# Performance work log

Measured on AMD Instinct MI355X. Metric: run time of the kernel, lower is better.

The kernel has to match this reference:

```python
import jax, jax.numpy as jnp
import numpy as np
from jax import lax

VOCAB = 100000; E = 512; HID = 1024; H = HID // 2; T = 7; L = 4096
START = 4; STOP = 5; NEG = -10000.0


def setup_inputs() -> dict:
    key = jax.random.key(0)
    ks = jax.random.split(key, 14)
    s = 0.05  # ~1/sqrt(H), matches torch default init scale
    transitions = jax.random.normal(ks[12], (T, T), dtype=jnp.float32)
    transitions = transitions.at[START, :].set(NEG).at[:, STOP].set(NEG)
    return {
        "sentence": jax.random.randint(ks[0], (L,), 0, VOCAB),
        "emb": jax.random.normal(ks[1], (VOCAB, E), dtype=jnp.float32) * s,
        "w_ih_f": jax.random.normal(ks[2], (4 * H, E), dtype=jnp.float32) * s,
        "w_hh_f": jax.random.normal(ks[3], (4 * H, H), dtype=jnp.float32) * s,
        "b_ih_f": jax.random.normal(ks[4], (4 * H,), dtype=jnp.float32) * s,
        "b_hh_f": jax.random.normal(ks[5], (4 * H,), dtype=jnp.float32) * s,
        "w_ih_b": jax.random.normal(ks[6], (4 * H, E), dtype=jnp.float32) * s,
        "w_hh_b": jax.random.normal(ks[7], (4 * H, H), dtype=jnp.float32) * s,
        "b_ih_b": jax.random.normal(ks[8], (4 * H,), dtype=jnp.float32) * s,
        "b_hh_b": jax.random.normal(ks[9], (4 * H,), dtype=jnp.float32) * s,
        "w_out": jax.random.normal(ks[10], (T, HID), dtype=jnp.float32) * s,
        "b_out": jax.random.normal(ks[11], (T,), dtype=jnp.float32) * s,
        "transitions": transitions,
    }


def _lstm_dir(x, w_ih, w_hh, b_ih, b_hh):
    # x: [L, E] -> hidden states [L, H]; zero initial state (torch default)
    xg = x @ w_ih.T + b_ih  # [L, 4H] precomputed input gates
    h0 = jnp.zeros((H,), x.dtype)
    c0 = jnp.zeros((H,), x.dtype)
    def step(carry, g):
        h, c = carry
        gates = g + w_hh @ h + b_hh
        i, f, gg, o = jnp.split(gates, 4)
        i = jax.nn.sigmoid(i); f = jax.nn.sigmoid(f)
        gg = jnp.tanh(gg); o = jax.nn.sigmoid(o)
        c = f * c + i * gg
        h = o * jnp.tanh(c)
        return (h, c), h
    _, hs = lax.scan(step, (h0, c0), xg)
    return hs


def reference(sentence, emb, w_ih_f, w_hh_f, b_ih_f, b_hh_f,
              w_ih_b, w_hh_b, b_ih_b, b_hh_b, w_out, b_out, transitions):
    x = emb[sentence]  # [L, E]
    hf = _lstm_dir(x, w_ih_f, w_hh_f, b_ih_f, b_hh_f)            # [L, H]
    hb = _lstm_dir(x[::-1], w_ih_b, w_hh_b, b_ih_b, b_hh_b)[::-1]
    feats = jnp.concatenate([hf, hb], axis=1) @ w_out.T + b_out  # [L, T]

    # Viterbi max-plus DP
    init = jnp.full((T,), NEG, feats.dtype).at[START].set(0.0)
    def vstep(fv, feat):
        sc = fv[None, :] + transitions           # [next, prev]
        bp = jnp.argmax(sc, axis=1)
        return jnp.max(sc, axis=1) + feat, bp
    fv, bptrs = lax.scan(vstep, init, feats)     # bptrs: [L, T]
    terminal = fv + transitions[STOP]
    best = jnp.argmax(terminal)
    score = terminal[best]
    # backtrack
    def bt(tag, bp):
        return bp[tag], tag
    _, path_rev = lax.scan(bt, best, bptrs[::-1])
    best_path = path_rev[::-1]                   # [L] tag ids
    return best_path, score
```

## Files before the change

### kernel.cpp

```cpp
#include <hip/hip_runtime.h>
#include <hip/hip_bf16.h>

#define L     4096
#define E     512
#define HID   1024
#define HH    512
#define G4    2048
#define T_TAG 7
#define START_TAG 4
#define STOP_TAG  5
#define NEGV  (-10000.0f)

#define NWRK  32
#define NHELP 224
#define NTILE (64 * 2 * 32)
#define SENT  0xFFFFFFFFu

__device__ __forceinline__ float aload_f(const float* p) {
    const unsigned int v = __hip_atomic_load((const unsigned int*)p,
                                             __ATOMIC_RELAXED,
                                             __HIP_MEMORY_SCOPE_AGENT);
    return __uint_as_float(v);
}
__device__ __forceinline__ void astore_f(float* p, float x) {
    __hip_atomic_store((unsigned int*)p, __float_as_uint(x),
                       __ATOMIC_RELAXED, __HIP_MEMORY_SCOPE_AGENT);
}

__global__ __launch_bounds__(512)
void fused_kernel(const int* __restrict__ sentence, const float* __restrict__ emb,
                  const float* __restrict__ wih_f, const float* __restrict__ bih_f,
                  const float* __restrict__ bhh_f,
                  const float* __restrict__ wih_b, const float* __restrict__ bih_b,
                  const float* __restrict__ bhh_b,
                  const float* __restrict__ whh_f, const float* __restrict__ whh_b,
                  const float* __restrict__ wout, const float* __restrict__ bout,
                  float* __restrict__ xg_f, float* __restrict__ xg_b,
                  float* __restrict__ hf, float* __restrict__ hb,
                  float* __restrict__ feats, int* cnt)
{
    const int bid = blockIdx.x;
    const int tid = threadIdx.x;

    __shared__ float h_lds[2][HH];
    __shared__ float glds[8][16];
    __shared__ float As[32][68];
    __shared__ float Bs[32][68];
    __shared__ int   sent_s[64];
    __shared__ float red_s[8][8];

    if (bid < NWRK) {
        const int dir = bid >> 4;
        const int rnk = bid & 15;

        const float* __restrict__ xg  = dir ? xg_b  : xg_f;
        const float* __restrict__ whh = dir ? whh_b : whh_f;
        float* __restrict__ hout = dir ? hb : hf;

        const int wave = tid >> 6;
        const int lane = tid & 63;
        const int g    = wave >> 1;
        const int jh   = wave & 1;
        const int u0   = rnk * 32;

        float w[16][8];
#pragma unroll
        for (int rr = 0; rr < 16; rr++) {
            const size_t row = (size_t)(g * HH + u0 + jh * 16 + rr);
#pragma unroll
            for (int k = 0; k < 8; k++)
                w[rr][k] = whh[row * HH + (size_t)(k * 64 + lane)];
        }

        float c_state = 0.f;
        const int uu = u0 + (tid & 31);

        auto wait_chunk = [&](int tc) {
            const int* cp = cnt + dir * 64 + tc;
            while (__hip_atomic_load(cp, __ATOMIC_ACQUIRE,
                                     __HIP_MEMORY_SCOPE_AGENT) < 32) {
                __builtin_amdgcn_s_sleep(1);
            }
        };

        float xq0 = 0.f, xq1 = 0.f, xq2 = 0.f, xq3 = 0.f;
        if (tid < 32) {
            wait_chunk(dir ? 63 : 0);
            const float* xgt = xg + (size_t)(dir ? (L - 1) : 0) * G4;
            xq0 = aload_f(xgt + uu);            xq1 = aload_f(xgt + HH + uu);
            xq2 = aload_f(xgt + 2 * HH + uu);   xq3 = aload_f(xgt + 3 * HH + uu);
        }

        for (int s = 0; s < L; s++) {
            const int t = dir ? (L - 1 - s) : s;
            const int p = s & 1;

            unsigned int v = 0;
            if (s > 0) {
                const int tp = dir ? (t + 1) : (t - 1);
                const unsigned int* hp =
                    (const unsigned int*)(hout + (size_t)tp * HH) + tid;
                do {
                    v = __hip_atomic_load(hp, __ATOMIC_RELAXED,
                                          __HIP_MEMORY_SCOPE_AGENT);
                } while (v == SENT);
            }
            h_lds[p][tid] = __uint_as_float(v);
            __syncthreads();

            float hv[8];
#pragma unroll
            for (int k = 0; k < 8; k++) hv[k] = h_lds[p][k * 64 + lane];

            float acc[16];
#pragma unroll
            for (int rr = 0; rr < 16; rr++) {
                float a = 0.f;
#pragma unroll
                for (int k = 0; k < 8; k++) a += w[rr][k] * hv[k];
                acc[rr] = a;
            }

            {
                const bool b0 = lane & 1;
#pragma unroll
                for (int r = 0; r < 8; r++) {
                    const float send = b0 ? acc[r] : acc[r + 8];
                    const float recv = __shfl_xor(send, 1, 64);
                    acc[r] = (b0 ? acc[r + 8] : acc[r]) + recv;
                }
                const bool b1 = lane & 2;
#pragma unroll
                for (int r = 0; r < 4; r++) {
                    const float send = b1 ? acc[r] : acc[r + 4];
                    const float recv = __shfl_xor(send, 2, 64);
                    acc[r] = (b1 ? acc[r + 4] : acc[r]) + recv;
                }
                const bool b2 = lane & 4;
#pragma unroll
                for (int r = 0; r < 2; r++) {
                    const float send = b2 ? acc[r] : acc[r + 2];
                    const float recv = __shfl_xor(send, 4, 64);
                    acc[r] = (b2 ? acc[r + 2] : acc[r]) + recv;
                }
                const bool b3 = lane & 8;
                {
                    const float send = b3 ? acc[0] : acc[1];
                    const float recv = __shfl_xor(send, 8, 64);
                    acc[0] = (b3 ? acc[1] : acc[0]) + recv;
                }
                acc[0] += __shfl_xor(acc[0], 16, 64);
                acc[0] += __shfl_xor(acc[0], 32, 64);
            }
            if (lane < 16) {
                const int R = ((lane & 1) << 3) | ((lane & 2) << 1) |
                              ((lane & 4) >> 1) | ((lane & 8) >> 3);
                glds[wave][R] = acc[0];
            }
            __syncthreads();

            if (tid < 32) {
                const int jh_ = tid >> 4;
                const int rr  = tid & 15;
                float iv = glds[0 + jh_][rr] + xq0;
                float fv = glds[2 + jh_][rr] + xq1;
                float gv = glds[4 + jh_][rr] + xq2;
                float ov = glds[6 + jh_][rr] + xq3;
                iv = 1.f / (1.f + expf(-iv));
                fv = 1.f / (1.f + expf(-fv));
                gv = tanhf(gv);
                ov = 1.f / (1.f + expf(-ov));
                c_state = fv * c_state + iv * gv;
                const float hval = ov * tanhf(c_state);
                __hip_atomic_store((unsigned int*)&hout[(size_t)t * HH + uu],
                                   __float_as_uint(hval), __ATOMIC_RELAXED,
                                   __HIP_MEMORY_SCOPE_AGENT);
                if (s + 1 < L) {
                    const int tn = dir ? (t - 1) : (t + 1);
                    if ((tn & 63) == (dir ? 63 : 0)) wait_chunk(tn >> 6);
                    const float* xgt = xg + (size_t)tn * G4;
                    xq0 = aload_f(xgt + uu);
                    xq1 = aload_f(xgt + HH + uu);
                    xq2 = aload_f(xgt + 2 * HH + uu);
                    xq3 = aload_f(xgt + 3 * HH + uu);
                }
            }
        }
        return;
    }

    const int hid_ = bid - NWRK;

    for (int tile = hid_; tile < NTILE; tile += NHELP) {
        const int jt = tile & 31;
        const int sd = tile >> 5;
        const int dr = sd & 1;
        const int sc = sd >> 1;
        const int t0 = dr ? (L - 64 - sc * 64) : (sc * 64);
        const int j0 = jt * 64;
        const float* __restrict__ wih = dr ? wih_b : wih_f;
        const float* __restrict__ bih = dr ? bih_b : bih_f;
        const float* __restrict__ bhh = dr ? bhh_b : bhh_f;
        float* __restrict__ xg = dr ? xg_b : xg_f;

        if (tid < 64) sent_s[tid] = sentence[t0 + tid];

        const int li = tid >> 3;
        const int k4 = (tid & 7) * 4;
        const int tx = tid & 15;
        const int ty = tid >> 4;

        float a00 = 0.f, a01 = 0.f, a02 = 0.f, a03 = 0.f;
        float a10 = 0.f, a11 = 0.f, a12 = 0.f, a13 = 0.f;

        for (int k0 = 0; k0 < E; k0 += 32) {
            __syncthreads();
            {
                const float4 av = *(const float4*)(emb + (size_t)sent_s[li] * E + k0 + k4);
                As[k4 + 0][li] = av.x; As[k4 + 1][li] = av.y;
                As[k4 + 2][li] = av.z; As[k4 + 3][li] = av.w;
                const float4 bv = *(const float4*)(wih + (size_t)(j0 + li) * E + k0 + k4);
                Bs[k4 + 0][li] = bv.x; Bs[k4 + 1][li] = bv.y;
                Bs[k4 + 2][li] = bv.z; Bs[k4 + 3][li] = bv.w;
            }
            __syncthreads();
#pragma unroll
            for (int k = 0; k < 32; k++) {
                const float a0 = As[k][ty * 2 + 0];
                const float a1 = As[k][ty * 2 + 1];
                const float4 b4 = *(const float4*)&Bs[k][tx * 4];
                a00 += a0 * b4.x; a01 += a0 * b4.y; a02 += a0 * b4.z; a03 += a0 * b4.w;
                a10 += a1 * b4.x; a11 += a1 * b4.y; a12 += a1 * b4.z; a13 += a1 * b4.w;
            }
        }

        {
            const int c0 = j0 + tx * 4;
            const float bsum0 = bih[c0 + 0] + bhh[c0 + 0];
            const float bsum1 = bih[c0 + 1] + bhh[c0 + 1];
            const float bsum2 = bih[c0 + 2] + bhh[c0 + 2];
            const float bsum3 = bih[c0 + 3] + bhh[c0 + 3];
            float* r0 = xg + (size_t)(t0 + ty * 2 + 0) * G4 + c0;
            float* r1 = xg + (size_t)(t0 + ty * 2 + 1) * G4 + c0;
            astore_f(r0 + 0, a00 + bsum0); astore_f(r0 + 1, a01 + bsum1);
            astore_f(r0 + 2, a02 + bsum2); astore_f(r0 + 3, a03 + bsum3);
            astore_f(r1 + 0, a10 + bsum0); astore_f(r1 + 1, a11 + bsum1);
            astore_f(r1 + 2, a12 + bsum2); astore_f(r1 + 3, a13 + bsum3);
        }
        __syncthreads();
        if (tid == 0)
            __hip_atomic_fetch_add(&cnt[dr * 64 + (t0 >> 6)], 1,
                                   __ATOMIC_RELEASE, __HIP_MEMORY_SCOPE_AGENT);
    }

    const int wave = tid >> 6, lane = tid & 63;
    for (int t = hid_; t < L; t += NHELP) {
        if (tid < 32) {
            const float* src = (tid < 16) ? hf : hb;
            const unsigned int* wp =
                (const unsigned int*)(src + (size_t)t * HH) + (tid & 15) * 32;
            while (__hip_atomic_load(wp, __ATOMIC_RELAXED,
                                     __HIP_MEMORY_SCOPE_AGENT) == SENT) {
                __builtin_amdgcn_s_sleep(8);
            }
        }
        __syncthreads();

        const unsigned int* p0 = (const unsigned int*)(hf + (size_t)t * HH) + tid;
        const unsigned int* p1 = (const unsigned int*)(hb + (size_t)t * HH) + tid;
        unsigned int v0, v1;
        do { v0 = __hip_atomic_load(p0, __ATOMIC_RELAXED,
                                    __HIP_MEMORY_SCOPE_AGENT); } while (v0 == SENT);
        do { v1 = __hip_atomic_load(p1, __ATOMIC_RELAXED,
                                    __HIP_MEMORY_SCOPE_AGENT); } while (v1 == SENT);
        const float x0 = __uint_as_float(v0);
        const float x1 = __uint_as_float(v1);

        float acc[T_TAG];
#pragma unroll
        for (int i = 0; i < T_TAG; i++)
            acc[i] = x0 * wout[i * HID + tid] + x1 * wout[i * HID + HH + tid];
#pragma unroll
        for (int m = 1; m < 64; m <<= 1) {
#pragma unroll
            for (int i = 0; i < T_TAG; i++) acc[i] += __shfl_xor(acc[i], m, 64);
        }
        if (lane == 0) {
#pragma unroll
            for (int i = 0; i < T_TAG; i++) red_s[wave][i] = acc[i];
        }
        __syncthreads();
        if (tid < T_TAG) {
            float ssum = bout[tid];
#pragma unroll
            for (int wv = 0; wv < 8; wv++) ssum += red_s[wv][tid];
            feats[(size_t)t * 8 + tid] = ssum;
        }
        __syncthreads();
    }
}

__global__ __launch_bounds__(64)
void viterbi_kernel(const float* __restrict__ feats, const float* __restrict__ trans,
                    float* __restrict__ out)
{
    __shared__ unsigned char bp[L][8];
    __shared__ unsigned char gl[64][8];
    __shared__ unsigned char bnd[64];

    const int tid = threadIdx.x;

    float tr[T_TAG][T_TAG];
#pragma unroll
    for (int i = 0; i < T_TAG; i++)
#pragma unroll
        for (int j = 0; j < T_TAG; j++) tr[i][j] = trans[i * T_TAG + j];

    const int d = tid % T_TAG;
    float trd[T_TAG];
#pragma unroll
    for (int j = 0; j < T_TAG; j++) trd[j] = trans[d * T_TAG + j];

    float trS[T_TAG];
#pragma unroll
    for (int j = 0; j < T_TAG; j++) trS[j] = trans[STOP_TAG * T_TAG + j];

    float fv0 = NEGV, fv1 = NEGV, fv2 = NEGV, fv3 = NEGV,
          fv4 = 0.f,  fv5 = NEGV, fv6 = NEGV;

    float4 qa[8], qb[8];
#pragma unroll
    for (int q = 0; q < 8; q++) {
        qa[q] = *(const float4*)(feats + (size_t)q * 8);
        qb[q] = *(const float4*)(feats + (size_t)q * 8 + 4);
    }

#define VMAXROW(I, OUT, FI)                                                    \
    {                                                                          \
        const float a0 = fv0 + tr[I][0], a1 = fv1 + tr[I][1];                  \
        const float a2 = fv2 + tr[I][2], a3 = fv3 + tr[I][3];                  \
        const float a4 = fv4 + tr[I][4], a5 = fv5 + tr[I][5];                  \
        const float a6 = fv6 + tr[I][6];                                       \
        const float m012 = fmaxf(fmaxf(a0, a1), a2);                           \
        const float m345 = fmaxf(fmaxf(a3, a4), a5);                           \
        OUT = fmaxf(fmaxf(m012, m345), a6) + (FI);                             \
    }

#define VSTEP(T, Q, PRE)                                                       \
    {                                                                          \
        const float4 fa = qa[Q], fb = qb[Q];                                   \
                     \
        {                                                                      \
            float bv_ = fv0 + trd[0]; int bj_ = 0; float c_;                   \
            c_ = fv1 + trd[1]; if (c_ > bv_) { bv_ = c_; bj_ = 1; }            \
            c_ = fv2 + trd[2]; if (c_ > bv_) { bv_ = c_; bj_ = 2; }            \
            c_ = fv3 + trd[3]; if (c_ > bv_) { bv_ = c_; bj_ = 3; }            \
            c_ = fv4 + trd[4]; if (c_ > bv_) { bv_ = c_; bj_ = 4; }            \
            c_ = fv5 + trd[5]; if (c_ > bv_) { bv_ = c_; bj_ = 5; }            \
            c_ = fv6 + trd[6]; if (c_ > bv_) { bv_ = c_; bj_ = 6; }            \
            if (tid < T_TAG) bp[(T)][tid] = (unsigned char)bj_;                \
        }                                                                      \
                 \
        float nf0, nf1, nf2, nf3, nf4, nf5, nf6;                               \
        VMAXROW(0, nf0, fa.x) VMAXROW(1, nf1, fa.y) VMAXROW(2, nf2, fa.z)      \
        VMAXROW(3, nf3, fa.w) VMAXROW(4, nf4, fb.x) VMAXROW(5, nf5, fb.y)      \
        VMAXROW(6, nf6, fb.z)                                                  \
        fv0 = nf0; fv1 = nf1; fv2 = nf2; fv3 = nf3;                            \
        fv4 = nf4; fv5 = nf5; fv6 = nf6;                                       \
        if (PRE) {                                                             \
            qa[Q] = *(const float4*)(feats + (size_t)((T) + 8) * 8);           \
            qb[Q] = *(const float4*)(feats + (size_t)((T) + 8) * 8 + 4);       \
        }                                                                      \
    }

    for (int tb = 0; tb < L - 8; tb += 8) {
#pragma unroll
        for (int q = 0; q < 8; q++) VSTEP(tb + q, q, true)
    }
    {
        const int tb = L - 8;
#pragma unroll
        for (int q = 0; q < 8; q++) VSTEP(tb + q, q, false)
    }
#undef VSTEP
#undef VMAXROW

    int bt_final; float best_score;
    {
        float bv_ = fv0 + trS[0]; int bj_ = 0; float c_;
        c_ = fv1 + trS[1]; if (c_ > bv_) { bv_ = c_; bj_ = 1; }
        c_ = fv2 + trS[2]; if (c_ > bv_) { bv_ = c_; bj_ = 2; }
        c_ = fv3 + trS[3]; if (c_ > bv_) { bv_ = c_; bj_ = 3; }
        c_ = fv4 + trS[4]; if (c_ > bv_) { bv_ = c_; bj_ = 4; }
        c_ = fv5 + trS[5]; if (c_ > bv_) { bv_ = c_; bj_ = 5; }
        c_ = fv6 + trS[6]; if (c_ > bv_) { bv_ = c_; bj_ = 6; }
        bt_final = bj_; best_score = bv_;
    }
    __syncthreads();

    const int lo = 64 * tid + 1;
    const int hi = (tid == 63) ? (L - 1) : (64 * tid + 64);
    {
        unsigned int c0 = 0, c1 = 1, c2 = 2, c3 = 3, c4 = 4, c5 = 5, c6 = 6;
        for (int t = hi; t >= lo; --t) {
            const unsigned char* row = &bp[t][0];
            c0 = row[c0]; c1 = row[c1]; c2 = row[c2]; c3 = row[c3];
            c4 = row[c4]; c5 = row[c5]; c6 = row[c6];
        }
        gl[tid][0] = (unsigned char)c0; gl[tid][1] = (unsigned char)c1;
        gl[tid][2] = (unsigned char)c2; gl[tid][3] = (unsigned char)c3;
        gl[tid][4] = (unsigned char)c4; gl[tid][5] = (unsigned char)c5;
        gl[tid][6] = (unsigned char)c6;
    }
    __syncthreads();

    if (tid == 0) {
        int b = bt_final;
        for (int l2 = 63; l2 >= 0; --l2) {
            bnd[l2] = (unsigned char)b;
            b = gl[l2][b];
        }
    }
    __syncthreads();

    {
        int tag = bnd[tid];
        for (int t = hi; t >= lo; --t) {
            tag = bp[t][tag];
            out[t - 1] = (float)tag;
        }
    }
    if (tid == 63) {
        out[L - 1] = (float)bt_final;
        out[L]     = best_score;
    }
}

extern "C" void kernel_launch(void* const* d_in, const int* in_sizes, int n_in,
                              void* d_out, int out_size, void* d_ws, size_t ws_size,
                              hipStream_t stream)
{
    const int*   sentence = (const int*)  d_in[0];
    const float* emb      = (const float*)d_in[1];
    const float* wih_f    = (const float*)d_in[2];
    const float* whh_f    = (const float*)d_in[3];
    const float* bih_f    = (const float*)d_in[4];
    const float* bhh_f    = (const float*)d_in[5];
    const float* wih_b    = (const float*)d_in[6];
    const float* whh_b    = (const float*)d_in[7];
    const float* bih_b    = (const float*)d_in[8];
    const float* bhh_b    = (const float*)d_in[9];
    const float* wout     = (const float*)d_in[10];
    const float* bout     = (const float*)d_in[11];
    const float* trans    = (const float*)d_in[12];
    float* out = (float*)d_out;

    char* ws = (char*)d_ws;
    int*   cnt    = (int*)ws;
    float* xg_f   = (float*)(ws + 1024);
    float* xg_b   = xg_f  + (size_t)L * G4;
    float* hfbuf  = xg_b  + (size_t)L * G4;
    float* hbbuf  = hfbuf + (size_t)L * HH;
    float* featsb = hbbuf + (size_t)L * HH;

    hipMemsetAsync(cnt, 0, 1024, stream);
    hipMemsetAsync(hfbuf, 0xFF, (size_t)2 * L * HH * sizeof(float), stream);

    void* args[] = { (void*)&sentence, (void*)&emb,
                     (void*)&wih_f, (void*)&bih_f, (void*)&bhh_f,
                     (void*)&wih_b, (void*)&bih_b, (void*)&bhh_b,
                     (void*)&whh_f, (void*)&whh_b,
                     (void*)&wout, (void*)&bout,
                     (void*)&xg_f, (void*)&xg_b,
                     (void*)&hfbuf, (void*)&hbbuf,
                     (void*)&featsb, (void*)&cnt };
    hipLaunchCooperativeKernel((void*)fused_kernel, dim3(NWRK + NHELP),
                               dim3(512), args, 0, stream);

    hipLaunchKernelGGL(viterbi_kernel, dim3(1), dim3(64), 0, stream,
                       featsb, trans, out);
}
```

Baseline: 9.102 ms.

## Fuse Viterbi into persistent kernel as dedicated block streaming feats via sentinels

Moves the Viterbi forward pass and backtrack into one block of the cooperative kernel. That block polls the feats buffer, which is pre-filled with a sentinel value, and double-buffers 32 timesteps at a time in LDS, so the DP overlaps the LSTM and feature computation instead of running after it in a second kernel launch. Shared memory becomes a union across the roles to fit the bp table, and one helper block is given up. The feats stores become atomic stores and the memset grows to cover feats. The trade-off is one fewer GEMM helper and spin-polling traffic from the Viterbi block.

```diff
diff --git a/kernel.cpp b/kernel.cpp
--- a/kernel.cpp
+++ b/kernel.cpp
@@ -12,20 +12,30 @@
 #define NEGV  (-10000.0f)
 
 #define NWRK  32
-#define NHELP 224
+#define VITB  32
+#define NHELP 223
 #define NTILE (64 * 2 * 32)
 #define SENT  0xFFFFFFFFu
 
+__device__ __forceinline__ unsigned int aload_u(const float* p) {
+    return __hip_atomic_load((const unsigned int*)p, __ATOMIC_RELAXED,
+                             __HIP_MEMORY_SCOPE_AGENT);
+}
 __device__ __forceinline__ float aload_f(const float* p) {
-    const unsigned int v = __hip_atomic_load((const unsigned int*)p,
-                                             __ATOMIC_RELAXED,
-                                             __HIP_MEMORY_SCOPE_AGENT);
-    return __uint_as_float(v);
+    return __uint_as_float(aload_u(p));
 }
 __device__ __forceinline__ void astore_f(float* p, float x) {
     __hip_atomic_store((unsigned int*)p, __float_as_uint(x),
                        __ATOMIC_RELAXED, __HIP_MEMORY_SCOPE_AGENT);
 }
+
+union SMem {
+    struct { float h_lds[2][HH]; float glds[8][16]; } wk;
+    struct { float As[32][68]; float Bs[32][68]; int sent[64];
+             float red[8][8]; } hp;
+    struct { unsigned char bp[L][8]; float stage[2][32][8];
+             unsigned char gl[64][8]; unsigned char bnd[64]; } vt;
+};
 
 __global__ __launch_bounds__(512)
 void fused_kernel(const int* __restrict__ sentence, const float* __restrict__ emb,
@@ -35,19 +45,15 @@
                   const float* __restrict__ bhh_b,
                   const float* __restrict__ whh_f, const float* __restrict__ whh_b,
                   const float* __restrict__ wout, const float* __restrict__ bout,
+                  const float* __restrict__ trans,
                   float* __restrict__ xg_f, float* __restrict__ xg_b,
                   float* __restrict__ hf, float* __restrict__ hb,
-                  float* __restrict__ feats, int* cnt)
+                  float* __restrict__ feats, float* __restrict__ out, int* cnt)
 {
     const int bid = blockIdx.x;
     const int tid = threadIdx.x;
 
-    __shared__ float h_lds[2][HH];
-    __shared__ float glds[8][16];
-    __shared__ float As[32][68];
-    __shared__ float Bs[32][68];
-    __shared__ int   sent_s[64];
-    __shared__ float red_s[8][8];
+    __shared__ SMem sm;
 
     if (bid < NWRK) {
         const int dir = bid >> 4;
@@ -105,12 +111,12 @@
                                           __HIP_MEMORY_SCOPE_AGENT);
                 } while (v == SENT);
             }
-            h_lds[p][tid] = __uint_as_float(v);
+            sm.wk.h_lds[p][tid] = __uint_as_float(v);
             __syncthreads();
 
             float hv[8];
 #pragma unroll
-            for (int k = 0; k < 8; k++) hv[k] = h_lds[p][k * 64 + lane];
+            for (int k = 0; k < 8; k++) hv[k] = sm.wk.h_lds[p][k * 64 + lane];
 
             float acc[16];
 #pragma unroll
@@ -155,17 +161,17 @@
             if (lane < 16) {
                 const int R = ((lane & 1) << 3) | ((lane & 2) << 1) |
                               ((lane & 4) >> 1) | ((lane & 8) >> 3);
-                glds[wave][R] = acc[0];
+                sm.wk.glds[wave][R] = acc[0];
             }
             __syncthreads();
 
             if (tid < 32) {
                 const int jh_ = tid >> 4;
                 const int rr  = tid & 15;
-                float iv = glds[0 + jh_][rr] + xq0;
-                float fv = glds[2 + jh_][rr] + xq1;
-                float gv = glds[4 + jh_][rr] + xq2;
-                float ov = glds[6 + jh_][rr] + xq3;
+                float iv = sm.wk.glds[0 + jh_][rr] + xq0;
+                float fv = sm.wk.glds[2 + jh_][rr] + xq1;
+                float gv = sm.wk.glds[4 + jh_][rr] + xq2;
+                float ov = sm.wk.glds[6 + jh_][rr] + xq3;
                 iv = 1.f / (1.f + expf(-iv));
                 fv = 1.f / (1.f + expf(-fv));
                 gv = tanhf(gv);
@@ -189,7 +195,169 @@
         return;
     }
 
-    const int hid_ = bid - NWRK;
+    if (bid == VITB) {
+        if (tid >= 64) return;
+
+        float tr[T_TAG][T_TAG];
+#pragma unroll
+        for (int i = 0; i < T_TAG; i++)
+#pragma unroll
+            for (int j = 0; j < T_TAG; j++) tr[i][j] = trans[i * T_TAG + j];
+
+        const int d = tid % T_TAG;
+        float trd[T_TAG];
+#pragma unroll
+        for (int j = 0; j < T_TAG; j++) trd[j] = trans[d * T_TAG + j];
+        float trS[T_TAG];
+#pragma unroll
+        for (int j = 0; j < T_TAG; j++) trS[j] = trans[STOP_TAG * T_TAG + j];
+
+        float fv0 = NEGV, fv1 = NEGV, fv2 = NEGV, fv3 = NEGV,
+              fv4 = 0.f,  fv5 = NEGV, fv6 = NEGV;
+
+        bool need[4];
+#pragma unroll
+        for (int k = 0; k < 4; k++) need[k] = (((tid * 4 + k) & 7) != 7);
+
+        {
+            unsigned int v[4] = { SENT, SENT, SENT, SENT };
+            int tries = 0;
+            for (;;) {
+                bool ok = true;
+#pragma unroll
+                for (int k = 0; k < 4; k++) {
+                    const int idx = tid * 4 + k;
+                    if (need[k] && v[k] == SENT)
+                        v[k] = aload_u(feats + (size_t)(idx >> 3) * 8 + (idx & 7));
+                    ok &= (!need[k]) || (v[k] != SENT);
+                }
+                if (ok) break;
+                if (++tries > 2) __builtin_amdgcn_s_sleep(16);
+            }
+#pragma unroll
+            for (int k = 0; k < 4; k++) {
+                const int idx = tid * 4 + k;
+                sm.vt.stage[0][idx >> 3][idx & 7] =
+                    need[k] ? __uint_as_float(v[k]) : 0.f;
+            }
+        }
+
+        unsigned int pf[4];
+#pragma unroll
+        for (int k = 0; k < 4; k++) {
+            const int idx = tid * 4 + k;
+            pf[k] = aload_u(feats + (size_t)(32 + (idx >> 3)) * 8 + (idx & 7));
+        }
+
+#define VMAXROW(I, OUT, FI)                                                    \
+        {                                                                      \
+            const float a0 = fv0 + tr[I][0], a1 = fv1 + tr[I][1];              \
+            const float a2 = fv2 + tr[I][2], a3 = fv3 + tr[I][3];              \
+            const float a4 = fv4 + tr[I][4], a5 = fv5 + tr[I][5];              \
+            const float a6 = fv6 + tr[I][6];                                   \
+            const float m012 = fmaxf(fmaxf(a0, a1), a2);                       \
+            const float m345 = fmaxf(fmaxf(a3, a4), a5);                       \
+            OUT = fmaxf(fmaxf(m012, m345), a6) + (FI);                         \
+        }
+
+        for (int b = 0; b < 128; b++) {
+            const int cur = b & 1;
+            const int t0 = b * 32;
+#pragma unroll 8
+            for (int q = 0; q < 32; q++) {
+                const int T = t0 + q;
+                const float4 fa = *(const float4*)&sm.vt.stage[cur][q][0];
+                const float4 fb = *(const float4*)&sm.vt.stage[cur][q][4];
+                {
+                    float bv_ = fv0 + trd[0]; int bj_ = 0; float c_;
+                    c_ = fv1 + trd[1]; if (c_ > bv_) { bv_ = c_; bj_ = 1; }
+                    c_ = fv2 + trd[2]; if (c_ > bv_) { bv_ = c_; bj_ = 2; }
+                    c_ = fv3 + trd[3]; if (c_ > bv_) { bv_ = c_; bj_ = 3; }
+                    c_ = fv4 + trd[4]; if (c_ > bv_) { bv_ = c_; bj_ = 4; }
+                    c_ = fv5 + trd[5]; if (c_ > bv_) { bv_ = c_; bj_ = 5; }
+                    c_ = fv6 + trd[6]; if (c_ > bv_) { bv_ = c_; bj_ = 6; }
+                    if (tid < T_TAG) sm.vt.bp[T][tid] = (unsigned char)bj_;
+                }
+                float nf0, nf1, nf2, nf3, nf4, nf5, nf6;
+                VMAXROW(0, nf0, fa.x) VMAXROW(1, nf1, fa.y) VMAXROW(2, nf2, fa.z)
+                VMAXROW(3, nf3, fa.w) VMAXROW(4, nf4, fb.x) VMAXROW(5, nf5, fb.y)
+                VMAXROW(6, nf6, fb.z)
+                fv0 = nf0; fv1 = nf1; fv2 = nf2; fv3 = nf3;
+                fv4 = nf4; fv5 = nf5; fv6 = nf6;
+            }
+            if (b + 1 < 128) {
+#pragma unroll
+                for (int k = 0; k < 4; k++) {
+                    const int idx = tid * 4 + k;
+                    if (need[k]) {
+                        while (pf[k] == SENT)
+                            pf[k] = aload_u(feats +
+                                    (size_t)((b + 1) * 32 + (idx >> 3)) * 8 + (idx & 7));
+                        sm.vt.stage[cur ^ 1][idx >> 3][idx & 7] = __uint_as_float(pf[k]);
+                    } else {
+                        sm.vt.stage[cur ^ 1][idx >> 3][idx & 7] = 0.f;
+                    }
+                }
+                if (b + 2 < 128) {
+#pragma unroll
+                    for (int k = 0; k < 4; k++) {
+                        const int idx = tid * 4 + k;
+                        pf[k] = aload_u(feats +
+                                (size_t)((b + 2) * 32 + (idx >> 3)) * 8 + (idx & 7));
+                    }
+                }
+            }
+        }
+#undef VMAXROW
+
+        int bt_final; float best_score;
+        {
+            float bv_ = fv0 + trS[0]; int bj_ = 0; float c_;
+            c_ = fv1 + trS[1]; if (c_ > bv_) { bv_ = c_; bj_ = 1; }
+            c_ = fv2 + trS[2]; if (c_ > bv_) { bv_ = c_; bj_ = 2; }
+            c_ = fv3 + trS[3]; if (c_ > bv_) { bv_ = c_; bj_ = 3; }
+            c_ = fv4 + trS[4]; if (c_ > bv_) { bv_ = c_; bj_ = 4; }
+            c_ = fv5 + trS[5]; if (c_ > bv_) { bv_ = c_; bj_ = 5; }
+            c_ = fv6 + trS[6]; if (c_ > bv_) { bv_ = c_; bj_ = 6; }
+            bt_final = bj_; best_score = bv_;
+        }
+
+        const int lo = 64 * tid + 1;
+        const int hi = (tid == 63) ? (L - 1) : (64 * tid + 64);
+        {
+            unsigned int c0 = 0, c1 = 1, c2 = 2, c3 = 3, c4 = 4, c5 = 5, c6 = 6;
+            for (int t = hi; t >= lo; --t) {
+                const unsigned char* row = &sm.vt.bp[t][0];
+                c0 = row[c0]; c1 = row[c1]; c2 = row[c2]; c3 = row[c3];
+                c4 = row[c4]; c5 = row[c5]; c6 = row[c6];
+            }
+            sm.vt.gl[tid][0] = (unsigned char)c0; sm.vt.gl[tid][1] = (unsigned char)c1;
+            sm.vt.gl[tid][2] = (unsigned char)c2; sm.vt.gl[tid][3] = (unsigned char)c3;
+            sm.vt.gl[tid][4] = (unsigned char)c4; sm.vt.gl[tid][5] = (unsigned char)c5;
+            sm.vt.gl[tid][6] = (unsigned char)c6;
+        }
+        if (tid == 0) {
+            int b = bt_final;
+            for (int l2 = 63; l2 >= 0; --l2) {
+                sm.vt.bnd[l2] = (unsigned char)b;
+                b = sm.vt.gl[l2][b];
+            }
+        }
+        {
+            int tag = sm.vt.bnd[tid];
+            for (int t = hi; t >= lo; --t) {
+                tag = sm.vt.bp[t][tag];
+                out[t - 1] = (float)tag;
+            }
+        }
+        if (tid == 63) {
+            out[L - 1] = (float)bt_final;
+            out[L]     = best_score;
+        }
+        return;
+    }
+
+    const int hid_ = bid - (NWRK + 1);
 
     for (int tile = hid_; tile < NTILE; tile += NHELP) {
         const int jt = tile & 31;
@@ -203,7 +371,7 @@
         const float* __restrict__ bhh = dr ? bhh_b : bhh_f;
         float* __restrict__ xg = dr ? xg_b : xg_f;
 
-        if (tid < 64) sent_s[tid] = sentence[t0 + tid];
+        if (tid < 64) sm.hp.sent[tid] = sentence[t0 + tid];
 
         const int li = tid >> 3;
         const int k4 = (tid & 7) * 4;
@@ -216,19 +384,19 @@
         for (int k0 = 0; k0 < E; k0 += 32) {
             __syncthreads();
             {
-                const float4 av = *(const float4*)(emb + (size_t)sent_s[li] * E + k0 + k4);
-                As[k4 + 0][li] = av.x; As[k4 + 1][li] = av.y;
-                As[k4 + 2][li] = av.z; As[k4 + 3][li] = av.w;
+                const float4 av = *(const float4*)(emb + (size_t)sm.hp.sent[li] * E + k0 + k4);
+                sm.hp.As[k4 + 0][li] = av.x; sm.hp.As[k4 + 1][li] = av.y;
+                sm.hp.As[k4 + 2][li] = av.z; sm.hp.As[k4 + 3][li] = av.w;
                 const float4 bv = *(const float4*)(wih + (size_t)(j0 + li) * E + k0 + k4);
-                Bs[k4 + 0][li] = bv.x; Bs[k4 + 1][li] = bv.y;
-                Bs[k4 + 2][li] = bv.z; Bs[k4 + 3][li] = bv.w;
+                sm.hp.Bs[k4 + 0][li] = bv.x; sm.hp.Bs[k4 + 1][li] = bv.y;
+                sm.hp.Bs[k4 + 2][li] = bv.z; sm.hp.Bs[k4 + 3][li] = bv.w;
             }
             __syncthreads();
 #pragma unroll
             for (int k = 0; k < 32; k++) {
-                const float a0 = As[k][ty * 2 + 0];
-                const float a1 = As[k][ty * 2 + 1];
-                const float4 b4 = *(const float4*)&Bs[k][tx * 4];
+                const float a0 = sm.hp.As[k][ty * 2 + 0];
+                const float a1 = sm.hp.As[k][ty * 2 + 1];
+                const float4 b4 = *(const float4*)&sm.hp.Bs[k][tx * 4];
                 a00 += a0 * b4.x; a01 += a0 * b4.y; a02 += a0 * b4.z; a03 += a0 * b4.w;
                 a10 += a1 * b4.x; a11 += a1 * b4.y; a12 += a1 * b4.z; a13 += a1 * b4.w;
             }
@@ -287,152 +455,19 @@
         }
         if (lane == 0) {
 #pragma unroll
-            for (int i = 0; i < T_TAG; i++) red_s[wave][i] = acc[i];
+            for (int i = 0; i < T_TAG; i++) sm.hp.red[wave][i] = acc[i];
         }
         __syncthreads();
-        if (tid < T_TAG) {
-            float ssum = bout[tid];
-#pragma unroll
-            for (int wv = 0; wv < 8; wv++) ssum += red_s[wv][tid];
-            feats[(size_t)t * 8 + tid] = ssum;
+        if (tid < 8) {
+            float ssum = 0.f;
+            if (tid < T_TAG) {
+                ssum = bout[tid];
+#pragma unroll
+                for (int wv = 0; wv < 8; wv++) ssum += sm.hp.red[wv][tid];
+            }
+            astore_f(&feats[(size_t)t * 8 + tid], ssum);
         }
         __syncthreads();
-    }
-}
-
-__global__ __launch_bounds__(64)
-void viterbi_kernel(const float* __restrict__ feats, const float* __restrict__ trans,
-                    float* __restrict__ out)
-{
-    __shared__ unsigned char bp[L][8];
-    __shared__ unsigned char gl[64][8];
-    __shared__ unsigned char bnd[64];
-
-    const int tid = threadIdx.x;
-
-    float tr[T_TAG][T_TAG];
-#pragma unroll
-    for (int i = 0; i < T_TAG; i++)
-#pragma unroll
-        for (int j = 0; j < T_TAG; j++) tr[i][j] = trans[i * T_TAG + j];
-
-    const int d = tid % T_TAG;
-    float trd[T_TAG];
-#pragma unroll
-    for (int j = 0; j < T_TAG; j++) trd[j] = trans[d * T_TAG + j];
-
-    float trS[T_TAG];
-#pragma unroll
-    for (int j = 0; j < T_TAG; j++) trS[j] = trans[STOP_TAG * T_TAG + j];
-
-    float fv0 = NEGV, fv1 = NEGV, fv2 = NEGV, fv3 = NEGV,
-          fv4 = 0.f,  fv5 = NEGV, fv6 = NEGV;
-
-    float4 qa[8], qb[8];
-#pragma unroll
-    for (int q = 0; q < 8; q++) {
-        qa[q] = *(const float4*)(feats + (size_t)q * 8);
-        qb[q] = *(const float4*)(feats + (size_t)q * 8 + 4);
-    }
-
-#define VMAXROW(I, OUT, FI)                                                    \
-    {                                                                          \
-        const float a0 = fv0 + tr[I][0], a1 = fv1 + tr[I][1];                  \
-        const float a2 = fv2 + tr[I][2], a3 = fv3 + tr[I][3];                  \
-        const float a4 = fv4 + tr[I][4], a5 = fv5 + tr[I][5];                  \
-        const float a6 = fv6 + tr[I][6];                                       \
-        const float m012 = fmaxf(fmaxf(a0, a1), a2);                           \
-        const float m345 = fmaxf(fmaxf(a3, a4), a5);                           \
-        OUT = fmaxf(fmaxf(m012, m345), a6) + (FI);                             \
-    }
-
-#define VSTEP(T, Q, PRE)                                                       \
-    {                                                                          \
-        const float4 fa = qa[Q], fb = qb[Q];                                   \
-                     \
-        {                                                                      \
-            float bv_ = fv0 + trd[0]; int bj_ = 0; float c_;                   \
-            c_ = fv1 + trd[1]; if (c_ > bv_) { bv_ = c_; bj_ = 1; }            \
-            c_ = fv2 + trd[2]; if (c_ > bv_) { bv_ = c_; bj_ = 2; }            \
-            c_ = fv3 + trd[3]; if (c_ > bv_) { bv_ = c_; bj_ = 3; }            \
-            c_ = fv4 + trd[4]; if (c_ > bv_) { bv_ = c_; bj_ = 4; }            \
-            c_ = fv5 + trd[5]; if (c_ > bv_) { bv_ = c_; bj_ = 5; }            \
-            c_ = fv6 + trd[6]; if (c_ > bv_) { bv_ = c_; bj_ = 6; }            \
-            if (tid < T_TAG) bp[(T)][tid] = (unsigned char)bj_;                \
-        }                                                                      \
-                 \
-        float nf0, nf1, nf2, nf3, nf4, nf5, nf6;                               \
-        VMAXROW(0, nf0, fa.x) VMAXROW(1, nf1, fa.y) VMAXROW(2, nf2, fa.z)      \
-        VMAXROW(3, nf3, fa.w) VMAXROW(4, nf4, fb.x) VMAXROW(5, nf5, fb.y)      \
-        VMAXROW(6, nf6, fb.z)                                                  \
-        fv0 = nf0; fv1 = nf1; fv2 = nf2; fv3 = nf3;                            \
-        fv4 = nf4; fv5 = nf5; fv6 = nf6;                                       \
-        if (PRE) {                                                             \
-            qa[Q] = *(const float4*)(feats + (size_t)((T) + 8) * 8);           \
-            qb[Q] = *(const float4*)(feats + (size_t)((T) + 8) * 8 + 4);       \
-        }                                                                      \
-    }
-
-    for (int tb = 0; tb < L - 8; tb += 8) {
-#pragma unroll
-        for (int q = 0; q < 8; q++) VSTEP(tb + q, q, true)
-    }
-    {
-        const int tb = L - 8;
-#pragma unroll
-        for (int q = 0; q < 8; q++) VSTEP(tb + q, q, false)
-    }
-#undef VSTEP
-#undef VMAXROW
-
-    int bt_final; float best_score;
-    {
-        float bv_ = fv0 + trS[0]; int bj_ = 0; float c_;
-        c_ = fv1 + trS[1]; if (c_ > bv_) { bv_ = c_; bj_ = 1; }
-        c_ = fv2 + trS[2]; if (c_ > bv_) { bv_ = c_; bj_ = 2; }
-        c_ = fv3 + trS[3]; if (c_ > bv_) { bv_ = c_; bj_ = 3; }
-        c_ = fv4 + trS[4]; if (c_ > bv_) { bv_ = c_; bj_ = 4; }
-        c_ = fv5 + trS[5]; if (c_ > bv_) { bv_ = c_; bj_ = 5; }
-        c_ = fv6 + trS[6]; if (c_ > bv_) { bv_ = c_; bj_ = 6; }
-        bt_final = bj_; best_score = bv_;
-    }
-    __syncthreads();
-
-    const int lo = 64 * tid + 1;
-    const int hi = (tid == 63) ? (L - 1) : (64 * tid + 64);
-    {
-        unsigned int c0 = 0, c1 = 1, c2 = 2, c3 = 3, c4 = 4, c5 = 5, c6 = 6;
-        for (int t = hi; t >= lo; --t) {
-            const unsigned char* row = &bp[t][0];
-            c0 = row[c0]; c1 = row[c1]; c2 = row[c2]; c3 = row[c3];
-            c4 = row[c4]; c5 = row[c5]; c6 = row[c6];
-        }
-        gl[tid][0] = (unsigned char)c0; gl[tid][1] = (unsigned char)c1;
-        gl[tid][2] = (unsigned char)c2; gl[tid][3] = (unsigned char)c3;
-        gl[tid][4] = (unsigned char)c4; gl[tid][5] = (unsigned char)c5;
-        gl[tid][6] = (unsigned char)c6;
-    }
-    __syncthreads();
-
-    if (tid == 0) {
-        int b = bt_final;
-        for (int l2 = 63; l2 >= 0; --l2) {
-            bnd[l2] = (unsigned char)b;
-            b = gl[l2][b];
-        }
-    }
-    __syncthreads();
-
-    {
-        int tag = bnd[tid];
-        for (int t = hi; t >= lo; --t) {
-            tag = bp[t][tag];
-            out[t - 1] = (float)tag;
-        }
-    }
-    if (tid == 63) {
-        out[L - 1] = (float)bt_final;
-        out[L]     = best_score;
     }
 }
 
@@ -464,19 +499,17 @@
     float* featsb = hbbuf + (size_t)L * HH;
 
     hipMemsetAsync(cnt, 0, 1024, stream);
-    hipMemsetAsync(hfbuf, 0xFF, (size_t)2 * L * HH * sizeof(float), stream);
+    hipMemsetAsync(hfbuf, 0xFF,
+                   ((size_t)2 * L * HH + (size_t)L * 8) * sizeof(float), stream);
 
     void* args[] = { (void*)&sentence, (void*)&emb,
                      (void*)&wih_f, (void*)&bih_f, (void*)&bhh_f,
                      (void*)&wih_b, (void*)&bih_b, (void*)&bhh_b,
                      (void*)&whh_f, (void*)&whh_b,
-                     (void*)&wout, (void*)&bout,
+                     (void*)&wout, (void*)&bout, (void*)&trans,
                      (void*)&xg_f, (void*)&xg_b,
                      (void*)&hfbuf, (void*)&hbbuf,
-                     (void*)&featsb, (void*)&cnt };
-    hipLaunchCooperativeKernel((void*)fused_kernel, dim3(NWRK + NHELP),
+                     (void*)&featsb, (void*)&out, (void*)&cnt };
+    hipLaunchCooperativeKernel((void*)fused_kernel, dim3(256),
                                dim3(512), args, 0, stream);
-
-    hipLaunchKernelGGL(viterbi_kernel, dim3(1), dim3(64), 0, stream,
-                       featsb, trans, out);
 }
```

After: 8.724 ms. 1.04x faster.
